# Kernel optimization log

Hardware: AMD Instinct MI355X
Metric: run time of the kernel (lower is better)

Reference implementation:

```python
import jax, jax.numpy as jnp
import numpy as np

H = 8          # num_heads
D_MODEL = 512  # hidden_dim
HEAD_DIM = D_MODEL // H
SCALE = HEAD_DIM ** -0.5
N = 4096
NUM_GRAPHS = 32
NEG_INF = jnp.float32(-jnp.inf)


def setup_inputs() -> dict:
    key = jax.random.key(0)
    ks = jax.random.split(key, 12)
    w_std = D_MODEL ** -0.5  # ~ torch Linear init scale
    inp = {
        "x": jax.random.normal(ks[0], (N, D_MODEL), jnp.float32),
        "attention_bias": jax.random.normal(ks[1], (H, N, N), jnp.float32),
        "batch": jnp.sort(jax.random.randint(ks[2], (N,), 0, NUM_GRAPHS)),
        "Wq": jax.random.normal(ks[3], (D_MODEL, D_MODEL), jnp.float32) * w_std,
        "bq": jax.random.normal(ks[4], (D_MODEL,), jnp.float32) * w_std,
        "Wk": jax.random.normal(ks[5], (D_MODEL, D_MODEL), jnp.float32) * w_std,
        "bk": jax.random.normal(ks[6], (D_MODEL,), jnp.float32) * w_std,
        "Wv": jax.random.normal(ks[7], (D_MODEL, D_MODEL), jnp.float32) * w_std,
        "bv": jax.random.normal(ks[8], (D_MODEL,), jnp.float32) * w_std,
        "Wo": jax.random.normal(ks[9], (D_MODEL, D_MODEL), jnp.float32) * w_std,
        "bo": jax.random.normal(ks[10], (D_MODEL,), jnp.float32) * w_std,
    }
    return inp


def reference(x, attention_bias, batch, Wq, bq, Wk, bk, Wv, bv, Wo, bo):
    n = x.shape[0]
    # projections (torch Linear: y = x @ W.T + b)
    q = (x @ Wq.T + bq).reshape(n, H, HEAD_DIM)
    k = (x @ Wk.T + bk).reshape(n, H, HEAD_DIM)
    v = (x @ Wv.T + bv).reshape(n, H, HEAD_DIM)
    # scores [H, N, N] with relative-PE bias
    attn = jnp.einsum("nhd,mhd->hnm", q, k) * SCALE + attention_bias
    # batch mask: attend only within the same graph
    batch_mask = batch[:, None] != batch[None, :]  # [N, N], True = masked
    attn = jnp.where(batch_mask[None, :, :], NEG_INF, attn)
    attn = jax.nn.softmax(attn, axis=-1)
    attn = jnp.nan_to_num(attn, nan=0.0)
    # dropout is identity in eval / dropout=0.0
    out = jnp.einsum("hnm,mhd->nhd", attn, v).reshape(n, D_MODEL)
    out = out @ Wo.T + bo
    return out
```

## Files before the change

### kernel.cpp

```cpp
#include <hip/hip_runtime.h>

#define NTOK 4096
#define DMODEL 512
#define NHEAD 8
#define HDIM 64
#define KDIM 512
#define KITER (KDIM / 64)

typedef __bf16 bf16x8 __attribute__((ext_vector_type(8)));
typedef float f32x4 __attribute__((ext_vector_type(4)));
typedef unsigned short u16x8 __attribute__((ext_vector_type(8)));
typedef unsigned short u16x4 __attribute__((ext_vector_type(4)));

#define NEGINF (-__builtin_inff())

__device__ __forceinline__ f32x4 mfma16(bf16x8 a, bf16x8 b, f32x4 c) {
  return __builtin_amdgcn_mfma_f32_16x16x32_bf16(a, b, c, 0, 0, 0);
}

__device__ __forceinline__ unsigned short f2bf(float f) {
  unsigned u = __builtin_bit_cast(unsigned, f);
  u += 0x7FFFu + ((u >> 16) & 1u);
  return (unsigned short)(u >> 16);
}

__device__ __forceinline__ void gload_lds16(const void* g, void* l) {
  __builtin_amdgcn_global_load_lds(
      (const __attribute__((address_space(1))) void*)g,
      (__attribute__((address_space(3))) void*)l, 16, 0, 0);
}

__global__ void convert_kernel(const float* __restrict__ x,
                               const float* __restrict__ Wq, const float* __restrict__ bq,
                               const float* __restrict__ Wk, const float* __restrict__ bk,
                               const float* __restrict__ Wv, const float* __restrict__ bv,
                               const float* __restrict__ Wo,
                               const int* __restrict__ batch,
                               unsigned short* __restrict__ xb,
                               unsigned short* __restrict__ wqkv,
                               unsigned short* __restrict__ wo,
                               float* __restrict__ bqkv,
                               int* __restrict__ qrange) {
  __shared__ int bsh[NTOK];
  if (blockIdx.x == 0) {
    for (int i = threadIdx.x; i < NTOK; i += 256) bsh[i] = batch[i];
  }
  const int XV = NTOK * DMODEL / 4;
  const int WV = DMODEL * DMODEL / 4;
  const int total = XV + 4 * WV + 1536 / 4;
  for (int i = blockIdx.x * blockDim.x + threadIdx.x; i < total;
       i += gridDim.x * blockDim.x) {
    if (i < XV) {
      float4 v = ((const float4*)x)[i];
      u16x4 pk = {f2bf(v.x), f2bf(v.y), f2bf(v.z), f2bf(v.w)};
      *(u16x4*)(xb + (size_t)i * 4) = pk;
    } else if (i < XV + 3 * WV) {
      int j = i - XV;
      const float* W; float sc; int jj;
      if (j < WV)          { W = Wq; sc = 0.125f; jj = j; }
      else if (j < 2 * WV) { W = Wk; sc = 1.0f;  jj = j - WV; }
      else                 { W = Wv; sc = 1.0f;  jj = j - 2 * WV; }
      float4 v = ((const float4*)W)[jj];
      u16x4 pk = {f2bf(v.x * sc), f2bf(v.y * sc), f2bf(v.z * sc), f2bf(v.w * sc)};
      *(u16x4*)(wqkv + (size_t)j * 4) = pk;
    } else if (i < XV + 4 * WV) {
      int j = i - XV - 3 * WV;
      float4 v = ((const float4*)Wo)[j];
      u16x4 pk = {f2bf(v.x), f2bf(v.y), f2bf(v.z), f2bf(v.w)};
      *(u16x4*)(wo + (size_t)j * 4) = pk;
    } else {
      int j = (i - XV - 4 * WV) * 4;
      #pragma unroll
      for (int t = 0; t < 4; ++t) {
        int e = j + t;
        float v = (e < 512) ? bq[e] * 0.125f
                 : (e < 1024 ? bk[e - 512] : bv[e - 1024]);
        bqkv[e] = v;
      }
    }
  }
  if (blockIdx.x == 0) {
    __syncthreads();
    if (threadIdx.x < 256) {
      int q0 = threadIdx.x * 16;
      int blo = bsh[q0];
      int bhi = bsh[q0 + 15];
      int lo = 0, hi = NTOK;
      while (lo < hi) { int m = (lo + hi) >> 1; if (bsh[m] < blo) lo = m + 1; else hi = m; }
      qrange[threadIdx.x * 2] = lo >> 6;
      lo = 0; hi = NTOK;
      while (lo < hi) { int m = (lo + hi) >> 1; if (bsh[m] < bhi + 1) lo = m + 1; else hi = m; }
      qrange[threadIdx.x * 2 + 1] = (lo + 63) >> 6;
    }
  }
}

template <int MODE>
__global__ __launch_bounds__(256, MODE ? 2 : 3) void gemm_kernel(
    const unsigned short* __restrict__ A,
    const unsigned short* __restrict__ B,
    const float* __restrict__ biasv,
    float* __restrict__ outf,
    unsigned short* __restrict__ qb,
    unsigned short* __restrict__ kb,
    unsigned short* __restrict__ vt) {
  constexpr int BM = MODE ? 64 : 128;
  constexpr int FM = MODE ? 2 : 4;
  constexpr int ALOADS = BM / 32;
  constexpr int BUFBYTES = (BM + 64) * 64 * 2;
  __shared__ __align__(16) unsigned short lds[(BM + 64) * 64 * 2];
  const int tid = threadIdx.x;
  const int lane = tid & 63;
  const int wv = tid >> 6;
  const int wm = wv >> 1, wn = wv & 1;
  const int r16 = lane & 15, g4 = lane >> 4;
  const int mt = blockIdx.x, nt = blockIdx.y;

  f32x4 acc[FM][2];
  #pragma unroll
  for (int i = 0; i < FM; ++i)
    #pragma unroll
    for (int j = 0; j < 2; ++j)
      acc[i][j] = (f32x4){0.f, 0.f, 0.f, 0.f};

  const int srow = tid >> 3;
  const int scolb = (tid & 7) << 4;

#define STAGE(KT, BI)                                                        \
  {                                                                          \
    char* bA = (char*)lds + (BI) * BUFBYTES;                                 \
    char* bB = bA + BM * 128;                                                \
    _Pragma("unroll") for (int i = 0; i < ALOADS; ++i) {                     \
      int row = i * 32 + srow;                                               \
      int cu_ = scolb ^ ((row & 7) << 4);                                    \
      gload_lds16(A + (size_t)(mt * BM + row) * KDIM + (KT) * 64 + (cu_ >> 1), \
                  bA + i * 4096 + wv * 1024);                                \
    }                                                                        \
    _Pragma("unroll") for (int i = 0; i < 2; ++i) {                          \
      int row = i * 32 + srow;                                               \
      int cu_ = scolb ^ ((row & 7) << 4);                                    \
      gload_lds16(B + (size_t)(nt * 64 + row) * KDIM + (KT) * 64 + (cu_ >> 1), \
                  bB + i * 4096 + wv * 1024);                                \
    }                                                                        \
  }

#define COMPUTE(BI)                                                          \
  {                                                                          \
    const char* base = (const char*)lds + (BI) * BUFBYTES;                   \
    _Pragma("unroll") for (int ks = 0; ks < 2; ++ks) {                       \
      bf16x8 af[FM], bfr[2];                                                 \
      _Pragma("unroll") for (int f = 0; f < FM; ++f) {                       \
        int ra = wm * (FM * 16) + f * 16 + r16;                              \
        af[f] = *(const bf16x8*)(base + ra * 128 +                           \
                                 ((ks * 64 + g4 * 16) ^ ((ra & 7) << 4)));   \
      }                                                                      \
      _Pragma("unroll") for (int f = 0; f < 2; ++f) {                        \
        int rb = wn * 32 + f * 16 + r16;                                     \
        bfr[f] = *(const bf16x8*)(base + BM * 128 + rb * 128 +               \
                                  ((ks * 64 + g4 * 16) ^ ((rb & 7) << 4)));  \
      }                                                                      \
      _Pragma("unroll") for (int fm = 0; fm < FM; ++fm)                      \
        _Pragma("unroll") for (int fn = 0; fn < 2; ++fn)                     \
          acc[fm][fn] = mfma16(af[fm], bfr[fn], acc[fm][fn]);                \
    }                                                                        \
  }

  STAGE(0, 0);
  #pragma unroll
  for (int kt = 0; kt < KITER; ++kt) {
    if (kt + 1 < KITER) {
      __builtin_amdgcn_s_barrier();
      STAGE(kt + 1, (kt + 1) & 1);
      if constexpr (MODE == 0)
        asm volatile("s_waitcnt vmcnt(6)" ::: "memory");
      else
        asm volatile("s_waitcnt vmcnt(4)" ::: "memory");
    } else {
      asm volatile("s_waitcnt vmcnt(0)" ::: "memory");
    }
    __builtin_amdgcn_s_barrier();
    COMPUTE(kt & 1);
  }
#undef STAGE
#undef COMPUTE

  #pragma unroll
  for (int fm = 0; fm < FM; ++fm) {
    #pragma unroll
    for (int fn = 0; fn < 2; ++fn) {
      int mb = mt * BM + wm * (FM * 16) + fm * 16 + g4 * 4;
      int n = nt * 64 + wn * 32 + fn * 16 + r16;
      float bv = biasv[n];
      if (MODE == 1) {
        #pragma unroll
        for (int r = 0; r < 4; ++r)
          outf[(size_t)(mb + r) * DMODEL + n] = acc[fm][fn][r] + bv;
      } else {
        if (n < 512) {
          #pragma unroll
          for (int r = 0; r < 4; ++r)
            qb[(size_t)(mb + r) * DMODEL + n] = f2bf(acc[fm][fn][r] + bv);
        } else if (n < 1024) {
          int nn = n - 512;
          #pragma unroll
          for (int r = 0; r < 4; ++r)
            kb[(size_t)(mb + r) * DMODEL + nn] = f2bf(acc[fm][fn][r] + bv);
        } else {
          int nn = n - 1024;
          u16x4 pk;
          #pragma unroll
          for (int r = 0; r < 4; ++r) pk[r] = f2bf(acc[fm][fn][r] + bv);
          *(u16x4*)(vt + (size_t)nn * NTOK + mb) = pk;
        }
      }
    }
  }
}

__global__ __launch_bounds__(64) void attn_kernel(
    const unsigned short* __restrict__ qb,
    const unsigned short* __restrict__ kb,
    const unsigned short* __restrict__ vt,
    const float* __restrict__ bias,
    const int* __restrict__ batch,
    const int* __restrict__ qrange,
    unsigned short* __restrict__ ao) {
  __shared__ __align__(16) unsigned short pl[16 * 72];
  const int lane = threadIdx.x & 63;
  const int r16 = lane & 15, g4 = lane >> 4;
  const int h = blockIdx.x & 7;
  const int qt = blockIdx.x >> 3;
  const int qrow0 = qt * 16;
  const int hoff = h * HDIM;

  const unsigned short* qrow = qb + (size_t)(qrow0 + r16) * DMODEL + hoff + g4 * 8;
  bf16x8 qa0 = *(const bf16x8*)qrow;
  bf16x8 qa1 = *(const bf16x8*)(qrow + 32);

  int qbt[4];
  const float* bprow[4];
  const float* bh = bias + (size_t)h * NTOK * NTOK;
  #pragma unroll
  for (int r = 0; r < 4; ++r) {
    qbt[r] = batch[qrow0 + g4 * 4 + r];
    bprow[r] = bh + (size_t)(qrow0 + g4 * 4 + r) * NTOK;
  }

  const int tile0 = qrange[qt * 2];
  const int tile1 = qrange[qt * 2 + 1];

  float m_r[4] = {NEGINF, NEGINF, NEGINF, NEGINF};
  float l_r[4] = {0.f, 0.f, 0.f, 0.f};
  f32x4 o[4];
  #pragma unroll
  for (int d = 0; d < 4; ++d) o[d] = (f32x4){0.f, 0.f, 0.f, 0.f};

#define PREFETCH_KB(T, K0, K1, BV, KBT)                                      \
  {                                                                          \
    int kvb_ = (T) << 6;                                                     \
    _Pragma("unroll") for (int c = 0; c < 4; ++c) {                          \
      const unsigned short* kp =                                             \
          kb + (size_t)(kvb_ + c * 16 + r16) * DMODEL + hoff + g4 * 8;       \
      K0[c] = *(const bf16x8*)kp;                                            \
      K1[c] = *(const bf16x8*)(kp + 32);                                     \
    }                                                                        \
    _Pragma("unroll") for (int c = 0; c < 4; ++c) {                          \
      KBT[c] = batch[kvb_ + c * 16 + r16];                                   \
      _Pragma("unroll") for (int r = 0; r < 4; ++r)                          \
        BV[c][r] = bprow[r][kvb_ + c * 16 + r16];                            \
    }                                                                        \
  }

#define TILE_STEP(T, K0C, K1C, BVC, KBTC, K0N, K1N, BVN, KBTN)               \
  {                                                                          \
    int kvb = (T) << 6;                                                      \
    f32x4 s[4];                                                              \
    __builtin_amdgcn_s_setprio(1);                                           \
    _Pragma("unroll") for (int c = 0; c < 4; ++c) {                          \
      f32x4 z = (f32x4){0.f, 0.f, 0.f, 0.f};                                 \
      z = mfma16(qa0, K0C[c], z);                                            \
      z = mfma16(qa1, K1C[c], z);                                            \
      s[c] = z;                                                              \
    }                                                                        \
    __builtin_amdgcn_s_setprio(0);                                           \
        \
    bf16x8 v0[4], v1[4];                                                     \
    _Pragma("unroll") for (int d = 0; d < 4; ++d) {                          \
      const unsigned short* vp =                                             \
          vt + (size_t)(hoff + d * 16 + r16) * NTOK + kvb + g4 * 8;          \
      v0[d] = *(const bf16x8*)vp;                                            \
      v1[d] = *(const bf16x8*)(vp + 32);                                     \
    }                                                                        \
     \
    {                                                                        \
      int tn_ = ((T) + 1 < tile1) ? (T) + 1 : (T);                           \
      PREFETCH_KB(tn_, K0N, K1N, BVN, KBTN);                                 \
    }                                                                        \
    _Pragma("unroll") for (int c = 0; c < 4; ++c)                            \
      _Pragma("unroll") for (int r = 0; r < 4; ++r)                          \
        s[c][r] = (qbt[r] == KBTC[c]) ? (s[c][r] + BVC[c][r]) : NEGINF;      \
    float scl[4];                                                            \
    _Pragma("unroll") for (int r = 0; r < 4; ++r) {                          \
      float tm = fmaxf(fmaxf(s[0][r], s[1][r]), fmaxf(s[2][r], s[3][r]));    \
      tm = fmaxf(tm, __shfl_xor(tm, 1));                                     \
      tm = fmaxf(tm, __shfl_xor(tm, 2));                                     \
      tm = fmaxf(tm, __shfl_xor(tm, 4));                                     \
      tm = fmaxf(tm, __shfl_xor(tm, 8));                                     \
      float mn = fmaxf(m_r[r], tm);                                          \
      bool dead = (mn == NEGINF);                                            \
      scl[r] = dead ? 1.0f : __expf(m_r[r] - mn);                            \
      m_r[r] = mn;                                                           \
      float rs = 0.f;                                                        \
      _Pragma("unroll") for (int c = 0; c < 4; ++c) {                        \
        float p = dead ? 0.0f : __expf(s[c][r] - mn);                        \
        s[c][r] = p;                                                         \
        rs += p;                                                             \
      }                                                                      \
      rs += __shfl_xor(rs, 1);                                               \
      rs += __shfl_xor(rs, 2);                                               \
      rs += __shfl_xor(rs, 4);                                               \
      rs += __shfl_xor(rs, 8);                                               \
      l_r[r] = l_r[r] * scl[r] + rs;                                         \
    }                                                                        \
    _Pragma("unroll") for (int c = 0; c < 4; ++c)                            \
      _Pragma("unroll") for (int r = 0; r < 4; ++r)                          \
        pl[(g4 * 4 + r) * 72 + c * 16 + r16] = f2bf(s[c][r]);                \
    asm volatile("" ::: "memory");                                           \
    u16x8 pr0 = *(const u16x8*)(pl + r16 * 72 + g4 * 8);                     \
    u16x8 pr1 = *(const u16x8*)(pl + r16 * 72 + 32 + g4 * 8);                \
    bf16x8 pa0 = __builtin_bit_cast(bf16x8, pr0);                            \
    bf16x8 pa1 = __builtin_bit_cast(bf16x8, pr1);                            \
    _Pragma("unroll") for (int d = 0; d < 4; ++d) {                          \
      _Pragma("unroll") for (int r = 0; r < 4; ++r) o[d][r] *= scl[r];       \
    }                                                                        \
    __builtin_amdgcn_s_setprio(1);                                           \
    _Pragma("unroll") for (int d = 0; d < 4; ++d) {                          \
      o[d] = mfma16(pa0, v0[d], o[d]);                                       \
      o[d] = mfma16(pa1, v1[d], o[d]);                                       \
    }                                                                        \
    __builtin_amdgcn_s_setprio(0);                                           \
  }

  bf16x8 ka0[4], ka1[4], kc0[4], kc1[4];
  float bva[4][4], bvb[4][4];
  int kta[4], ktb[4];
  PREFETCH_KB(tile0, ka0, ka1, bva, kta);
  int t = tile0;
  while (true) {
    TILE_STEP(t, ka0, ka1, bva, kta, kc0, kc1, bvb, ktb);
    if (++t >= tile1) break;
    TILE_STEP(t, kc0, kc1, bvb, ktb, ka0, ka1, bva, kta);
    if (++t >= tile1) break;
  }

  #pragma unroll
  for (int r = 0; r < 4; ++r) {
    float inv = (l_r[r] > 0.f) ? 1.0f / l_r[r] : 0.0f;
    #pragma unroll
    for (int d = 0; d < 4; ++d)
      ao[(size_t)(qrow0 + g4 * 4 + r) * DMODEL + hoff + d * 16 + r16] =
          f2bf(o[d][r] * inv);
  }
#undef PREFETCH_KB
#undef TILE_STEP
}

extern "C" void kernel_launch(void* const* d_in, const int* in_sizes, int n_in,
                              void* d_out, int out_size, void* d_ws, size_t ws_size,
                              hipStream_t stream) {
  const float* x  = (const float*)d_in[0];
  const float* ab = (const float*)d_in[1];
  const int* batch = (const int*)d_in[2];
  const float* Wq = (const float*)d_in[3];
  const float* bq = (const float*)d_in[4];
  const float* Wk = (const float*)d_in[5];
  const float* bk = (const float*)d_in[6];
  const float* Wv = (const float*)d_in[7];
  const float* bv = (const float*)d_in[8];
  const float* Wo = (const float*)d_in[9];
  const float* bo = (const float*)d_in[10];
  float* out = (float*)d_out;

  char* ws = (char*)d_ws;
  const size_t MB = 1024 * 1024;
  unsigned short* xb   = (unsigned short*)(ws);
  unsigned short* qb   = (unsigned short*)(ws + 4 * MB);
  unsigned short* kb   = (unsigned short*)(ws + 8 * MB);
  unsigned short* vt   = (unsigned short*)(ws + 12 * MB);
  unsigned short* aout = (unsigned short*)(ws + 16 * MB);
  unsigned short* wqkv = (unsigned short*)(ws + 20 * MB);
  unsigned short* wo   = (unsigned short*)(ws + 22 * MB);
  float* bqkv          = (float*)(ws + 23 * MB);
  int* qrange          = (int*)(ws + 23 * MB + 65536);

  convert_kernel<<<dim3(1024), dim3(256), 0, stream>>>(
      x, Wq, bq, Wk, bk, Wv, bv, Wo, batch, xb, wqkv, wo, bqkv, qrange);

  gemm_kernel<0><<<dim3(32, 24), dim3(256), 0, stream>>>(
      xb, wqkv, bqkv, nullptr, qb, kb, vt);

  attn_kernel<<<dim3(2048), dim3(64), 0, stream>>>(
      qb, kb, vt, ab, batch, qrange, aout);

  gemm_kernel<1><<<dim3(64, 8), dim3(256), 0, stream>>>(
      aout, wo, bo, out, nullptr, nullptr, nullptr);
}
```

Measured before the change: 51.65 us.

## Fuse four pipeline stages into one cooperative persistent kernel with grid syncs

Merges the convert, QKV GEMM, attention and output GEMM kernels into one cooperative launch of 256 persistent blocks, separated by grid-wide syncs. The goal is to remove per-kernel launch overhead and the tail gaps between kernels. The cost is lower parallelism: 256 blocks replace grids of 768, 2048 and 512. Attention tasks now run as four waves per 256-thread block instead of single-wave blocks, so occupancy and latency hiding may drop. If the cooperative launch fails, it falls back to the original four launches.

```diff
diff --git a/kernel.cpp b/kernel.cpp
--- a/kernel.cpp
+++ b/kernel.cpp
@@ -1,4 +1,7 @@
 #include <hip/hip_runtime.h>
+#include <hip/hip_cooperative_groups.h>
+
+namespace cg = cooperative_groups;
 
 #define NTOK 4096
 #define DMODEL 512
@@ -6,6 +9,7 @@
 #define HDIM 64
 #define KDIM 512
 #define KITER (KDIM / 64)
+#define NBLK 256
 
 typedef __bf16 bf16x8 __attribute__((ext_vector_type(8)));
 typedef float f32x4 __attribute__((ext_vector_type(4)));
@@ -30,26 +34,23 @@
       (__attribute__((address_space(3))) void*)l, 16, 0, 0);
 }
 
-__global__ void convert_kernel(const float* __restrict__ x,
-                               const float* __restrict__ Wq, const float* __restrict__ bq,
-                               const float* __restrict__ Wk, const float* __restrict__ bk,
-                               const float* __restrict__ Wv, const float* __restrict__ bv,
-                               const float* __restrict__ Wo,
-                               const int* __restrict__ batch,
-                               unsigned short* __restrict__ xb,
-                               unsigned short* __restrict__ wqkv,
-                               unsigned short* __restrict__ wo,
-                               float* __restrict__ bqkv,
-                               int* __restrict__ qrange) {
-  __shared__ int bsh[NTOK];
+__device__ __forceinline__ void convert_phase(
+    const float* __restrict__ x,
+    const float* __restrict__ Wq, const float* __restrict__ bq,
+    const float* __restrict__ Wk, const float* __restrict__ bk,
+    const float* __restrict__ Wv, const float* __restrict__ bv,
+    const float* __restrict__ Wo, const int* __restrict__ batch,
+    unsigned short* __restrict__ xb, unsigned short* __restrict__ wqkv,
+    unsigned short* __restrict__ wo, float* __restrict__ bqkv,
+    int* __restrict__ qrange, int* bsh) {
   if (blockIdx.x == 0) {
-    for (int i = threadIdx.x; i < NTOK; i += 256) bsh[i] = batch[i];
+    for (int i = threadIdx.x; i < NTOK; i += blockDim.x) bsh[i] = batch[i];
   }
   const int XV = NTOK * DMODEL / 4;
   const int WV = DMODEL * DMODEL / 4;
   const int total = XV + 4 * WV + 1536 / 4;
-  for (int i = blockIdx.x * blockDim.x + threadIdx.x; i < total;
-       i += gridDim.x * blockDim.x) {
+  const int stride = gridDim.x * blockDim.x;
+  for (int i = blockIdx.x * blockDim.x + threadIdx.x; i < total; i += stride) {
     if (i < XV) {
       float4 v = ((const float4*)x)[i];
       u16x4 pk = {f2bf(v.x), f2bf(v.y), f2bf(v.z), f2bf(v.w)};
@@ -92,29 +93,29 @@
       while (lo < hi) { int m = (lo + hi) >> 1; if (bsh[m] < bhi + 1) lo = m + 1; else hi = m; }
       qrange[threadIdx.x * 2 + 1] = (lo + 63) >> 6;
     }
+    __syncthreads();
   }
 }
 
 template <int MODE>
-__global__ __launch_bounds__(256, MODE ? 2 : 3) void gemm_kernel(
+__device__ __forceinline__ void gemm_tile(
     const unsigned short* __restrict__ A,
     const unsigned short* __restrict__ B,
     const float* __restrict__ biasv,
     float* __restrict__ outf,
     unsigned short* __restrict__ qb,
     unsigned short* __restrict__ kb,
-    unsigned short* __restrict__ vt) {
+    unsigned short* __restrict__ vt,
+    int mt, int nt, unsigned short* lds) {
   constexpr int BM = MODE ? 64 : 128;
   constexpr int FM = MODE ? 2 : 4;
   constexpr int ALOADS = BM / 32;
   constexpr int BUFBYTES = (BM + 64) * 64 * 2;
-  __shared__ __align__(16) unsigned short lds[(BM + 64) * 64 * 2];
   const int tid = threadIdx.x;
   const int lane = tid & 63;
   const int wv = tid >> 6;
   const int wm = wv >> 1, wn = wv & 1;
   const int r16 = lane & 15, g4 = lane >> 4;
-  const int mt = blockIdx.x, nt = blockIdx.y;
 
   f32x4 acc[FM][2];
   #pragma unroll
@@ -165,6 +166,8 @@
     }                                                                        \
   }
 
+  asm volatile("s_waitcnt vmcnt(0)" ::: "memory");
+  __syncthreads();
   STAGE(0, 0);
   #pragma unroll
   for (int kt = 0; kt < KITER; ++kt) {
@@ -217,19 +220,17 @@
   }
 }
 
-__global__ __launch_bounds__(64) void attn_kernel(
+__device__ __forceinline__ void attn_task(
     const unsigned short* __restrict__ qb,
     const unsigned short* __restrict__ kb,
     const unsigned short* __restrict__ vt,
     const float* __restrict__ bias,
     const int* __restrict__ batch,
     const int* __restrict__ qrange,
-    unsigned short* __restrict__ ao) {
-  __shared__ __align__(16) unsigned short pl[16 * 72];
+    unsigned short* __restrict__ ao,
+    int h, int qt, unsigned short* pl) {
   const int lane = threadIdx.x & 63;
   const int r16 = lane & 15, g4 = lane >> 4;
-  const int h = blockIdx.x & 7;
-  const int qt = blockIdx.x >> 3;
   const int qrow0 = qt * 16;
   const int hoff = h * HDIM;
 
@@ -283,7 +284,6 @@
       s[c] = z;                                                              \
     }                                                                        \
     __builtin_amdgcn_s_setprio(0);                                           \
-        \
     bf16x8 v0[4], v1[4];                                                     \
     _Pragma("unroll") for (int d = 0; d < 4; ++d) {                          \
       const unsigned short* vp =                                             \
@@ -291,7 +291,6 @@
       v0[d] = *(const bf16x8*)vp;                                            \
       v1[d] = *(const bf16x8*)(vp + 32);                                     \
     }                                                                        \
-     \
     {                                                                        \
       int tn_ = ((T) + 1 < tile1) ? (T) + 1 : (T);                           \
       PREFETCH_KB(tn_, K0N, K1N, BVN, KBTN);                                 \
@@ -365,43 +364,104 @@
 #undef TILE_STEP
 }
 
+struct FusedArgs {
+  const float* x; const float* ab; const int* batch;
+  const float* Wq; const float* bq; const float* Wk; const float* bk;
+  const float* Wv; const float* bv; const float* Wo; const float* bo;
+  float* out;
+  unsigned short* xb; unsigned short* qb; unsigned short* kb;
+  unsigned short* vt; unsigned short* aout; unsigned short* wqkv;
+  unsigned short* wo; float* bqkv; int* qrange;
+};
+
+__global__ __launch_bounds__(256, 2) void fused_kernel(FusedArgs a) {
+  __shared__ __align__(16) unsigned char uLDS[49152];
+  cg::grid_group grid = cg::this_grid();
+
+  convert_phase(a.x, a.Wq, a.bq, a.Wk, a.bk, a.Wv, a.bv, a.Wo, a.batch,
+                a.xb, a.wqkv, a.wo, a.bqkv, a.qrange, (int*)uLDS);
+  grid.sync();
+
+  for (int t = blockIdx.x; t < 768; t += NBLK)
+    gemm_tile<0>(a.xb, a.wqkv, a.bqkv, nullptr, a.qb, a.kb, a.vt,
+                 t & 31, t >> 5, (unsigned short*)uLDS);
+  grid.sync();
+
+  {
+    unsigned short* pl = (unsigned short*)uLDS + (threadIdx.x >> 6) * (16 * 72);
+    int wid = blockIdx.x * 4 + (threadIdx.x >> 6);
+    for (int task = wid; task < 2048; task += NBLK * 4)
+      attn_task(a.qb, a.kb, a.vt, a.ab, a.batch, a.qrange, a.aout,
+                task & 7, task >> 3, pl);
+  }
+  grid.sync();
+
+  for (int t = blockIdx.x; t < 512; t += NBLK)
+    gemm_tile<1>(a.aout, a.wo, a.bo, a.out, nullptr, nullptr, nullptr,
+                 t & 63, t >> 6, (unsigned short*)uLDS);
+}
+
+__global__ void convert_kernel_w(FusedArgs a) {
+  __shared__ int bsh[NTOK];
+  convert_phase(a.x, a.Wq, a.bq, a.Wk, a.bk, a.Wv, a.bv, a.Wo, a.batch,
+                a.xb, a.wqkv, a.wo, a.bqkv, a.qrange, bsh);
+}
+
+template <int MODE>
+__global__ __launch_bounds__(256, MODE ? 2 : 3) void gemm_kernel_w(FusedArgs a) {
+  constexpr int BM = MODE ? 64 : 128;
+  __shared__ __align__(16) unsigned short lds[(BM + 64) * 64 * 2];
+  if (MODE == 0)
+    gemm_tile<0>(a.xb, a.wqkv, a.bqkv, nullptr, a.qb, a.kb, a.vt,
+                 blockIdx.x, blockIdx.y, lds);
+  else
+    gemm_tile<1>(a.aout, a.wo, a.bo, a.out, nullptr, nullptr, nullptr,
+                 blockIdx.x, blockIdx.y, lds);
+}
+
+__global__ __launch_bounds__(64) void attn_kernel_w(FusedArgs a) {
+  __shared__ __align__(16) unsigned short pl[16 * 72];
+  attn_task(a.qb, a.kb, a.vt, a.ab, a.batch, a.qrange, a.aout,
+            blockIdx.x & 7, blockIdx.x >> 3, pl);
+}
+
 extern "C" void kernel_launch(void* const* d_in, const int* in_sizes, int n_in,
                               void* d_out, int out_size, void* d_ws, size_t ws_size,
                               hipStream_t stream) {
-  const float* x  = (const float*)d_in[0];
-  const float* ab = (const float*)d_in[1];
-  const int* batch = (const int*)d_in[2];
-  const float* Wq = (const float*)d_in[3];
-  const float* bq = (const float*)d_in[4];
-  const float* Wk = (const float*)d_in[5];
-  const float* bk = (const float*)d_in[6];
-  const float* Wv = (const float*)d_in[7];
-  const float* bv = (const float*)d_in[8];
-  const float* Wo = (const float*)d_in[9];
-  const float* bo = (const float*)d_in[10];
-  float* out = (float*)d_out;
-
   char* ws = (char*)d_ws;
   const size_t MB = 1024 * 1024;
-  unsigned short* xb   = (unsigned short*)(ws);
-  unsigned short* qb   = (unsigned short*)(ws + 4 * MB);
-  unsigned short* kb   = (unsigned short*)(ws + 8 * MB);
-  unsigned short* vt   = (unsigned short*)(ws + 12 * MB);
-  unsigned short* aout = (unsigned short*)(ws + 16 * MB);
-  unsigned short* wqkv = (unsigned short*)(ws + 20 * MB);
-  unsigned short* wo   = (unsigned short*)(ws + 22 * MB);
-  float* bqkv          = (float*)(ws + 23 * MB);
-  int* qrange          = (int*)(ws + 23 * MB + 65536);
-
-  convert_kernel<<<dim3(1024), dim3(256), 0, stream>>>(
-      x, Wq, bq, Wk, bk, Wv, bv, Wo, batch, xb, wqkv, wo, bqkv, qrange);
-
-  gemm_kernel<0><<<dim3(32, 24), dim3(256), 0, stream>>>(
-      xb, wqkv, bqkv, nullptr, qb, kb, vt);
-
-  attn_kernel<<<dim3(2048), dim3(64), 0, stream>>>(
-      qb, kb, vt, ab, batch, qrange, aout);
-
-  gemm_kernel<1><<<dim3(64, 8), dim3(256), 0, stream>>>(
-      aout, wo, bo, out, nullptr, nullptr, nullptr);
-}
+
+  FusedArgs a;
+  a.x  = (const float*)d_in[0];
+  a.ab = (const float*)d_in[1];
+  a.batch = (const int*)d_in[2];
+  a.Wq = (const float*)d_in[3];
+  a.bq = (const float*)d_in[4];
+  a.Wk = (const float*)d_in[5];
+  a.bk = (const float*)d_in[6];
+  a.Wv = (const float*)d_in[7];
+  a.bv = (const float*)d_in[8];
+  a.Wo = (const float*)d_in[9];
+  a.bo = (const float*)d_in[10];
+  a.out = (float*)d_out;
+  a.xb   = (unsigned short*)(ws);
+  a.qb   = (unsigned short*)(ws + 4 * MB);
+  a.kb   = (unsigned short*)(ws + 8 * MB);
+  a.vt   = (unsigned short*)(ws + 12 * MB);
+  a.aout = (unsigned short*)(ws + 16 * MB);
+  a.wqkv = (unsigned short*)(ws + 20 * MB);
+  a.wo   = (unsigned short*)(ws + 22 * MB);
+  a.bqkv   = (float*)(ws + 23 * MB);
+  a.qrange = (int*)(ws + 23 * MB + 65536);
+
+  void* kp[] = {&a};
+  hipError_t err = hipLaunchCooperativeKernel(
+      (void*)fused_kernel, dim3(NBLK), dim3(256), kp, 0, stream);
+
+  if (err != hipSuccess) {
+    convert_kernel_w<<<dim3(1024), dim3(256), 0, stream>>>(a);
+    gemm_kernel_w<0><<<dim3(32, 24), dim3(256), 0, stream>>>(a);
+    attn_kernel_w<<<dim3(2048), dim3(64), 0, stream>>>(a);
+    gemm_kernel_w<1><<<dim3(64, 8), dim3(256), 0, stream>>>(a);
+  }
+}
```

New measurement: 156.4 us. 3.03x slower.
